# Performance work log

Measured on AMD Instinct MI355X. Metric: run time of the kernel, lower is better.

## Reference

```python
import jax, jax.numpy as jnp
import numpy as np

T, B, D, H = 512, 512, 512, 512

def setup_inputs() -> dict:
    key = jax.random.key(0)
    k_in, k_wih, k_whh, k_bih, k_bhh = jax.random.split(key, 5)
    s = 1.0 / np.sqrt(H)  # torch RNNCell init scale
    return {
        "inputs": jax.random.normal(k_in, (T, B, D), dtype=jnp.float32),
        "W_ih": jax.random.uniform(k_wih, (H, D), jnp.float32, -s, s),
        "W_hh": jax.random.uniform(k_whh, (H, H), jnp.float32, -s, s),
        "b_ih": jax.random.uniform(k_bih, (H,), jnp.float32, -s, s),
        "b_hh": jax.random.uniform(k_bhh, (H,), jnp.float32, -s, s),
        "hidden_size": H,
    }

def reference(inputs, W_ih, W_hh, b_ih, b_hh, hidden_size):
    # h_{t+1} = tanh(x_t @ W_ih^T + b_ih + h_t @ W_hh^T + b_hh)
    # Original inits hidden with inputs.shape[0] rows (quirk: requires T == B).
    h0 = jnp.zeros((inputs.shape[0], hidden_size), dtype=inputs.dtype)
    # Precompute the input projection for all steps in one big GEMM;
    # the recurrence itself must remain sequential.
    xp = jnp.einsum("tbd,hd->tbh", inputs, W_ih) + b_ih + b_hh  # [T, B, H]

    def step(h, xp_t):
        h = jnp.tanh(xp_t + h @ W_hh.T)
        return h, None

    h_final, _ = jax.lax.scan(step, h0, xp)
    return h_final
```

## Files before the change

kernel.cpp:

```cpp
#include <hip/hip_runtime.h>
#include <stdint.h>

#define TSTEPS 512
#define NB 512
#define ND 512
#define NH 512

#define WPG 32
#define NGROUPS 32
#define CTR_STRIDE 64

typedef _Float16 half8 __attribute__((ext_vector_type(8)));
typedef float float4v __attribute__((ext_vector_type(4)));

__device__ __forceinline__ float fast_tanh(float x) {
  float e = __expf(2.0f * x);
  return 1.0f - 2.0f * __builtin_amdgcn_rcpf(e + 1.0f);
}

__global__ void __launch_bounds__(256, 1)
rnn_persistent(const float* __restrict__ x,
               const float* __restrict__ Wih,
               const float* __restrict__ Whh,
               const float* __restrict__ bih,
               const float* __restrict__ bhh,
               float* __restrict__ out,
               _Float16* __restrict__ hbuf,
               unsigned* __restrict__ counters)
{
  __shared__ __attribute__((aligned(16))) float red[4][16][68];

  const int bid  = blockIdx.x;
  const int grp  = bid & 31;
  const int cwg  = bid >> 5;
  const int wave = threadIdx.x >> 6;
  const int lane = threadIdx.x & 63;
  const int m    = lane & 15;
  const int quad = lane >> 4;
  const int tid  = threadIdx.x;

  const int R     = grp * 16;
  const int C0    = cwg * 64;
  const int kbase = wave * 128;

  unsigned* ctr = counters + grp * CTR_STRIDE;

  half8 wih_f[4][4];
  half8 whh_f[4][4];
  #pragma unroll
  for (int tile = 0; tile < 4; ++tile) {
    const int n = C0 + tile * 16 + m;
    const float* wr_ih = Wih + (size_t)n * ND;
    const float* wr_hh = Whh + (size_t)n * NH;
    #pragma unroll
    for (int kk = 0; kk < 4; ++kk) {
      const int k0 = kbase + kk * 32 + quad * 8;
      half8 a, b;
      #pragma unroll
      for (int j = 0; j < 8; ++j) {
        a[j] = (_Float16)wr_ih[k0 + j];
        b[j] = (_Float16)wr_hh[k0 + j];
      }
      wih_f[kk][tile] = a;
      whh_f[kk][tile] = b;
    }
  }

  const int prow = tid >> 4;
  const int pcol = (tid & 15) * 4;
  float4v bias4;
  #pragma unroll
  for (int j = 0; j < 4; ++j)
    bias4[j] = bih[C0 + pcol + j] + bhh[C0 + pcol + j];

  const int myrow = R + m;
  const int orow  = quad * 4;

  for (int t = 0; t < TSTEPS; ++t) {
    float4v acc[4];
    #pragma unroll
    for (int tile = 0; tile < 4; ++tile) acc[tile] = (float4v){0.f, 0.f, 0.f, 0.f};

    const float* xrow = x + ((size_t)t * NB + myrow) * ND + kbase + quad * 8;
    float4v xv[4][2];
    #pragma unroll
    for (int kk = 0; kk < 4; ++kk) {
      xv[kk][0] = *(const float4v*)(xrow + kk * 32);
      xv[kk][1] = *(const float4v*)(xrow + kk * 32 + 4);
    }
    #pragma unroll
    for (int kk = 0; kk < 4; ++kk) {
      half8 a;
      #pragma unroll
      for (int j = 0; j < 4; ++j) {
        a[j]     = (_Float16)xv[kk][0][j];
        a[j + 4] = (_Float16)xv[kk][1][j];
      }
      #pragma unroll
      for (int tile = 0; tile < 4; ++tile)
        acc[tile] = __builtin_amdgcn_mfma_f32_16x16x32_f16(a, wih_f[kk][tile], acc[tile], 0, 0, 0);
    }

    if (t > 0) {
      const unsigned tgt = (unsigned)(WPG * t);
      unsigned c;
      while ((c = __hip_atomic_load(ctr, __ATOMIC_RELAXED, __HIP_MEMORY_SCOPE_AGENT)) < tgt)
        __builtin_amdgcn_s_sleep(1);
      const _Float16* hb = hbuf + (size_t)(t & 1) * NB * NH + (size_t)(c >> 31);
      const unsigned long long* hrow =
          (const unsigned long long*)(hb + (size_t)myrow * NH + kbase + quad * 8);
      #pragma unroll
      for (int kk = 0; kk < 4; ++kk) {
        unsigned long long lo = __hip_atomic_load(hrow + kk * 8,     __ATOMIC_RELAXED, __HIP_MEMORY_SCOPE_AGENT);
        unsigned long long hi = __hip_atomic_load(hrow + kk * 8 + 1, __ATOMIC_RELAXED, __HIP_MEMORY_SCOPE_AGENT);
        union { unsigned long long u[2]; half8 h; } cv;
        cv.u[0] = lo; cv.u[1] = hi;
        #pragma unroll
        for (int tile = 0; tile < 4; ++tile)
          acc[tile] = __builtin_amdgcn_mfma_f32_16x16x32_f16(cv.h, whh_f[kk][tile], acc[tile], 0, 0, 0);
      }
    }

    #pragma unroll
    for (int tile = 0; tile < 4; ++tile) {
      #pragma unroll
      for (int r = 0; r < 4; ++r)
        red[wave][orow + r][tile * 16 + m] = acc[tile][r];
    }
    __syncthreads();
    float4v s = bias4;
    #pragma unroll
    for (int w = 0; w < 4; ++w) {
      const float4v v = *(const float4v*)&red[w][prow][pcol];
      s[0] += v[0]; s[1] += v[1]; s[2] += v[2]; s[3] += v[3];
    }
    float4v o;
    #pragma unroll
    for (int j = 0; j < 4; ++j) o[j] = fast_tanh(s[j]);

    if (t < TSTEPS - 1) {
      _Float16* hb1 = hbuf + (size_t)((t + 1) & 1) * NB * NH;
      union { _Float16 h[4]; unsigned long long u; } pk;
      #pragma unroll
      for (int j = 0; j < 4; ++j) pk.h[j] = (_Float16)o[j];
      __hip_atomic_store(
          (unsigned long long*)(hb1 + (size_t)(R + prow) * NH + C0 + pcol),
          pk.u, __ATOMIC_RELAXED, __HIP_MEMORY_SCOPE_AGENT);
      asm volatile("s_waitcnt vmcnt(0)" ::: "memory");
      if (lane == 0)
        __hip_atomic_fetch_add(ctr, 1u, __ATOMIC_RELAXED, __HIP_MEMORY_SCOPE_AGENT);
    } else {
      *(float4v*)(out + (size_t)(R + prow) * NH + C0 + pcol) = o;
    }
  }
}

extern "C" void kernel_launch(void* const* d_in, const int* in_sizes, int n_in,
                              void* d_out, int out_size, void* d_ws, size_t ws_size,
                              hipStream_t stream) {
  const float* x   = (const float*)d_in[0];
  const float* Wih = (const float*)d_in[1];
  const float* Whh = (const float*)d_in[2];
  const float* bih = (const float*)d_in[3];
  const float* bhh = (const float*)d_in[4];
  float* out = (float*)d_out;

  _Float16* hbuf     = (_Float16*)d_ws;
  unsigned* counters = (unsigned*)((char*)d_ws + (size_t)2 * NB * NH * 2);

  (void)hipMemsetAsync(counters, 0, NGROUPS * CTR_STRIDE * sizeof(unsigned), stream);

  rnn_persistent<<<dim3(256), dim3(256), 0, stream>>>(
      x, Wih, Whh, bih, bhh, out, hbuf, counters);
}
```

Before: 2.563 ms.

## Replace shared atomic counter with per-block step flags and prefetch next input

Each block now publishes the step it has finished to its own padded flag cell with a plain store, replacing the fetch-add on a counter shared by the whole group. Consumers poll the 8 flag cells in parallel across lanes and leave the wait once every lane sees the target. This removes contention on one atomic address, at the cost of an extra __syncthreads per step before the flag store. The x rows for step t+1 are also loaded during step t, double-buffered in registers, so global load latency overlaps the recurrence wait.

Result: faster. 2.193 ms (-14.4%).

```diff
diff --git a/kernel.cpp b/kernel.cpp
--- a/kernel.cpp
+++ b/kernel.cpp
@@ -6,9 +6,8 @@
 #define ND 512
 #define NH 512
 
-#define WPG 32
 #define NGROUPS 32
-#define CTR_STRIDE 64
+#define CELL_STRIDE 64
 
 typedef _Float16 half8 __attribute__((ext_vector_type(8)));
 typedef float float4v __attribute__((ext_vector_type(4)));
@@ -26,7 +25,7 @@
                const float* __restrict__ bhh,
                float* __restrict__ out,
                _Float16* __restrict__ hbuf,
-               unsigned* __restrict__ counters)
+               unsigned* __restrict__ flags)
 {
   __shared__ __attribute__((aligned(16))) float red[4][16][68];
 
@@ -43,7 +42,9 @@
   const int C0    = cwg * 64;
   const int kbase = wave * 128;
 
-  unsigned* ctr = counters + grp * CTR_STRIDE;
+  unsigned* gflags = flags + (size_t)grp * 8 * CELL_STRIDE;
+  unsigned* myflag = gflags + cwg * CELL_STRIDE;
+  const unsigned* pollcell = gflags + ((wave << 1) | (lane & 1)) * CELL_STRIDE;
 
   half8 wih_f[4][4];
   half8 whh_f[4][4];
@@ -76,83 +77,110 @@
   const int myrow = R + m;
   const int orow  = quad * 4;
 
-  for (int t = 0; t < TSTEPS; ++t) {
-    float4v acc[4];
-    #pragma unroll
-    for (int tile = 0; tile < 4; ++tile) acc[tile] = (float4v){0.f, 0.f, 0.f, 0.f};
-
-    const float* xrow = x + ((size_t)t * NB + myrow) * ND + kbase + quad * 8;
-    float4v xv[4][2];
+  float4v xvA[4][2], xvB[4][2];
+  {
+    const float* xrow0 = x + (size_t)myrow * ND + kbase + quad * 8;
     #pragma unroll
     for (int kk = 0; kk < 4; ++kk) {
-      xv[kk][0] = *(const float4v*)(xrow + kk * 32);
-      xv[kk][1] = *(const float4v*)(xrow + kk * 32 + 4);
+      xvA[kk][0] = *(const float4v*)(xrow0 + kk * 32);
+      xvA[kk][1] = *(const float4v*)(xrow0 + kk * 32 + 4);
     }
-    #pragma unroll
-    for (int kk = 0; kk < 4; ++kk) {
-      half8 a;
-      #pragma unroll
-      for (int j = 0; j < 4; ++j) {
-        a[j]     = (_Float16)xv[kk][0][j];
-        a[j + 4] = (_Float16)xv[kk][1][j];
-      }
-      #pragma unroll
-      for (int tile = 0; tile < 4; ++tile)
-        acc[tile] = __builtin_amdgcn_mfma_f32_16x16x32_f16(a, wih_f[kk][tile], acc[tile], 0, 0, 0);
-    }
-
-    if (t > 0) {
-      const unsigned tgt = (unsigned)(WPG * t);
-      unsigned c;
-      while ((c = __hip_atomic_load(ctr, __ATOMIC_RELAXED, __HIP_MEMORY_SCOPE_AGENT)) < tgt)
-        __builtin_amdgcn_s_sleep(1);
-      const _Float16* hb = hbuf + (size_t)(t & 1) * NB * NH + (size_t)(c >> 31);
-      const unsigned long long* hrow =
-          (const unsigned long long*)(hb + (size_t)myrow * NH + kbase + quad * 8);
-      #pragma unroll
-      for (int kk = 0; kk < 4; ++kk) {
-        unsigned long long lo = __hip_atomic_load(hrow + kk * 8,     __ATOMIC_RELAXED, __HIP_MEMORY_SCOPE_AGENT);
-        unsigned long long hi = __hip_atomic_load(hrow + kk * 8 + 1, __ATOMIC_RELAXED, __HIP_MEMORY_SCOPE_AGENT);
-        union { unsigned long long u[2]; half8 h; } cv;
-        cv.u[0] = lo; cv.u[1] = hi;
-        #pragma unroll
-        for (int tile = 0; tile < 4; ++tile)
-          acc[tile] = __builtin_amdgcn_mfma_f32_16x16x32_f16(cv.h, whh_f[kk][tile], acc[tile], 0, 0, 0);
-      }
-    }
-
-    #pragma unroll
-    for (int tile = 0; tile < 4; ++tile) {
-      #pragma unroll
-      for (int r = 0; r < 4; ++r)
-        red[wave][orow + r][tile * 16 + m] = acc[tile][r];
-    }
-    __syncthreads();
-    float4v s = bias4;
-    #pragma unroll
-    for (int w = 0; w < 4; ++w) {
-      const float4v v = *(const float4v*)&red[w][prow][pcol];
-      s[0] += v[0]; s[1] += v[1]; s[2] += v[2]; s[3] += v[3];
-    }
-    float4v o;
-    #pragma unroll
-    for (int j = 0; j < 4; ++j) o[j] = fast_tanh(s[j]);
-
-    if (t < TSTEPS - 1) {
-      _Float16* hb1 = hbuf + (size_t)((t + 1) & 1) * NB * NH;
-      union { _Float16 h[4]; unsigned long long u; } pk;
-      #pragma unroll
-      for (int j = 0; j < 4; ++j) pk.h[j] = (_Float16)o[j];
-      __hip_atomic_store(
-          (unsigned long long*)(hb1 + (size_t)(R + prow) * NH + C0 + pcol),
-          pk.u, __ATOMIC_RELAXED, __HIP_MEMORY_SCOPE_AGENT);
-      asm volatile("s_waitcnt vmcnt(0)" ::: "memory");
-      if (lane == 0)
-        __hip_atomic_fetch_add(ctr, 1u, __ATOMIC_RELAXED, __HIP_MEMORY_SCOPE_AGENT);
-    } else {
-      *(float4v*)(out + (size_t)(R + prow) * NH + C0 + pcol) = o;
-    }
-  }
+  }
+
+#define STEP(T, XU, XP)                                                        \
+  {                                                                            \
+    const int t_ = (T);                                                        \
+    float4v acc[4];                                                            \
+    _Pragma("unroll")                                                          \
+    for (int tile = 0; tile < 4; ++tile) acc[tile] = (float4v){0.f,0.f,0.f,0.f};\
+                       \
+    _Pragma("unroll")                                                          \
+    for (int kk = 0; kk < 4; ++kk) {                                           \
+      half8 a;                                                                 \
+      _Pragma("unroll")                                                        \
+      for (int j = 0; j < 4; ++j) {                                            \
+        a[j]     = (_Float16)XU[kk][0][j];                                     \
+        a[j + 4] = (_Float16)XU[kk][1][j];                                     \
+      }                                                                        \
+      _Pragma("unroll")                                                        \
+      for (int tile = 0; tile < 4; ++tile)                                     \
+        acc[tile] = __builtin_amdgcn_mfma_f32_16x16x32_f16(a, wih_f[kk][tile], acc[tile], 0, 0, 0); \
+    }                                                                          \
+         \
+    {                                                                          \
+      const int tn_ = (t_ + 1 < TSTEPS) ? (t_ + 1) : t_;                       \
+      const float* xrow_ = x + ((size_t)tn_ * NB + myrow) * ND + kbase + quad * 8; \
+      _Pragma("unroll")                                                        \
+      for (int kk = 0; kk < 4; ++kk) {                                         \
+        XP[kk][0] = *(const float4v*)(xrow_ + kk * 32);                        \
+        XP[kk][1] = *(const float4v*)(xrow_ + kk * 32 + 4);                    \
+      }                                                                        \
+    }                                                                          \
+          \
+    if (t_ > 0) {                                                              \
+      const unsigned tgt = (unsigned)t_;                                       \
+      unsigned v;                                                              \
+      for (;;) {                                                               \
+        v = __hip_atomic_load(pollcell, __ATOMIC_RELAXED, __HIP_MEMORY_SCOPE_AGENT); \
+        if (__all((int)(v >= tgt))) break;                                     \
+        __builtin_amdgcn_s_sleep(1);                                           \
+      }                                                                        \
+        \
+      const unsigned v2 = (unsigned)__shfl_xor((int)v, 1, 64);                 \
+      const _Float16* hb = hbuf + (size_t)(t_ & 1) * NB * NH + (size_t)((v | v2) >> 31); \
+      const unsigned long long* hrow =                                         \
+          (const unsigned long long*)(hb + (size_t)myrow * NH + kbase + quad * 8); \
+      _Pragma("unroll")                                                        \
+      for (int kk = 0; kk < 4; ++kk) {                                         \
+        unsigned long long lo = __hip_atomic_load(hrow + kk * 8,     __ATOMIC_RELAXED, __HIP_MEMORY_SCOPE_AGENT); \
+        unsigned long long hi = __hip_atomic_load(hrow + kk * 8 + 1, __ATOMIC_RELAXED, __HIP_MEMORY_SCOPE_AGENT); \
+        union { unsigned long long u[2]; half8 h; } cv;                        \
+        cv.u[0] = lo; cv.u[1] = hi;                                            \
+        _Pragma("unroll")                                                      \
+        for (int tile = 0; tile < 4; ++tile)                                   \
+          acc[tile] = __builtin_amdgcn_mfma_f32_16x16x32_f16(cv.h, whh_f[kk][tile], acc[tile], 0, 0, 0); \
+      }                                                                        \
+    }                                                                          \
+                                           \
+    _Pragma("unroll")                                                          \
+    for (int tile = 0; tile < 4; ++tile) {                                     \
+      _Pragma("unroll")                                                        \
+      for (int r = 0; r < 4; ++r)                                              \
+        red[wave][orow + r][tile * 16 + m] = acc[tile][r];                     \
+    }                                                                          \
+    __syncthreads();                                           \
+    float4v s = bias4;                                                         \
+    _Pragma("unroll")                                                          \
+    for (int w = 0; w < 4; ++w) {                                              \
+      const float4v vv = *(const float4v*)&red[w][prow][pcol];                 \
+      s[0] += vv[0]; s[1] += vv[1]; s[2] += vv[2]; s[3] += vv[3];              \
+    }                                                                          \
+    float4v o;                                                                 \
+    _Pragma("unroll")                                                          \
+    for (int j = 0; j < 4; ++j) o[j] = fast_tanh(s[j]);                        \
+    if (t_ < TSTEPS - 1) {                                                     \
+      _Float16* hb1 = hbuf + (size_t)((t_ + 1) & 1) * NB * NH;                 \
+      union { _Float16 h[4]; unsigned long long u; } pk;                       \
+      _Pragma("unroll")                                                        \
+      for (int j = 0; j < 4; ++j) pk.h[j] = (_Float16)o[j];                    \
+      __hip_atomic_store(                                                      \
+          (unsigned long long*)(hb1 + (size_t)(R + prow) * NH + C0 + pcol),    \
+          pk.u, __ATOMIC_RELAXED, __HIP_MEMORY_SCOPE_AGENT);                   \
+        \
+      asm volatile("s_waitcnt vmcnt(0)" ::: "memory");                         \
+      __syncthreads();   \
+      if (tid == 0)                                                            \
+        __hip_atomic_store(myflag, (unsigned)(t_ + 1), __ATOMIC_RELAXED, __HIP_MEMORY_SCOPE_AGENT); \
+    } else {                                                                   \
+      *(float4v*)(out + (size_t)(R + prow) * NH + C0 + pcol) = o;              \
+    }                                                                          \
+  }
+
+  for (int t = 0; t < TSTEPS; t += 2) {
+    STEP(t,     xvA, xvB);
+    STEP(t + 1, xvB, xvA);
+  }
+#undef STEP
 }
 
 extern "C" void kernel_launch(void* const* d_in, const int* in_sizes, int n_in,
@@ -165,11 +193,13 @@
   const float* bhh = (const float*)d_in[4];
   float* out = (float*)d_out;
 
-  _Float16* hbuf     = (_Float16*)d_ws;
-  unsigned* counters = (unsigned*)((char*)d_ws + (size_t)2 * NB * NH * 2);
-
-  (void)hipMemsetAsync(counters, 0, NGROUPS * CTR_STRIDE * sizeof(unsigned), stream);
+  _Float16* hbuf  = (_Float16*)d_ws;
+  unsigned* flags = (unsigned*)((char*)d_ws + (size_t)2 * NB * NH * 2);
+
+  (void)hipMemsetAsync(flags, 0,
+                       (size_t)NGROUPS * 8 * CELL_STRIDE * sizeof(unsigned),
+                       stream);
 
   rnn_persistent<<<dim3(256), dim3(256), 0, stream>>>(
-      x, Wih, Whh, bih, bhh, out, hbuf, counters);
+      x, Wih, Whh, bih, bhh, out, hbuf, flags);
 }
```
